# Kernel optimization log

Hardware: AMD Instinct MI355X
Metric: run time of the kernel (lower is better)

Reference implementation:

```python
import jax, jax.numpy as jnp
import numpy as np

DIM = 768
NUM_HEADS = 12
DECAY_RATE = 5.0


def setup_inputs() -> dict:
    key = jax.random.key(0)
    k1, k2, k3, k4 = jax.random.split(key, 4)
    B, N, C = 4, 1024, DIM
    x = jax.random.normal(k1, (B, N, C), dtype=jnp.float32)
    # torch nn.Linear weights: y = x @ W.T ; qkv_bias=False
    qkv_w = jax.random.normal(k2, (3 * C, C), dtype=jnp.float32) * (1.0 / np.sqrt(C))
    proj_w = jax.random.normal(k3, (C, C), dtype=jnp.float32) * (1.0 / np.sqrt(C))
    proj_b = jax.random.normal(k4, (C,), dtype=jnp.float32) * 0.01
    return {"x": x, "qkv_w": qkv_w, "proj_w": proj_w, "proj_b": proj_b, "cur_epoch": 3}


def reference(x, qkv_w, proj_w, proj_b, cur_epoch):
    B, N, C = x.shape
    H = NUM_HEADS
    hd = C // H
    scale = hd ** -0.5

    qkv = (x @ qkv_w.T).reshape(B, N, 3, H, hd).transpose(2, 0, 3, 1, 4)  # [3,B,H,N,hd]
    q, k, v = qkv[0], qkv[1], qkv[2]

    scores = jnp.einsum("bhqd,bhkd->bhqk", q, k) * scale
    logp = jax.nn.log_softmax(scores, axis=-1)
    attn = jnp.exp(logp)  # [B,H,N,N]

    # Per-key entropy: column j of attn flattened over (B,H,N) is renormalized
    # by Categorical; dividing by num_heads cancels under normalization.
    # H(p/s) = log(s) - (1/s) * sum(p * log p)
    s = jnp.sum(attn, axis=(0, 1, 2))                 # [N]
    plogp = jnp.sum(attn * logp, axis=(0, 1, 2))      # [N]
    entropies = jnp.log(s) - plogp / s

    # threshold decay: factor = sum_{i=0}^{cur_epoch-1} decay*exp(-(i+1))
    factor = DECAY_RATE * float(np.sum(np.exp(-(np.arange(cur_epoch) + 1.0))))
    entropy_threshold = float(np.log(C)) - factor

    # attn[:,:,:,keep] @ v[:,:,keep,:] == (attn * mask) @ v  (zeroed columns drop out)
    mask = (entropies <= entropy_threshold).astype(attn.dtype)  # [N]
    out = jnp.einsum("bhqk,bhkd->bhqd", attn * mask[None, None, None, :], v)
    out = out.transpose(0, 2, 1, 3).reshape(B, N, C)
    out = out @ proj_w.T + proj_b
    return out
```

## Files before the change

### kernel.cpp

```cpp
#include <hip/hip_runtime.h>


typedef __bf16 bf16x8 __attribute__((ext_vector_type(8)));
typedef __bf16 bf16x4 __attribute__((ext_vector_type(4)));
typedef float  f32x4  __attribute__((ext_vector_type(4)));

#define MFMA16(a, b, c) __builtin_amdgcn_mfma_f32_16x16x32_bf16((a), (b), (c), 0, 0, 0)
#define LOG2E_8 0.18033688f

__global__ __launch_bounds__(256) void kc_conv(
    const float* __restrict__ x, const float* __restrict__ qw, const float* __restrict__ pw,
    __bf16* __restrict__ xb, __bf16* __restrict__ qwb, __bf16* __restrict__ pwb,
    float* __restrict__ colSP, int* __restrict__ keepCnt)
{
  const int i = blockIdx.x * 256 + threadIdx.x;
  const float4* src;
  __bf16* dst;
  int j;
  if (i < 786432)       { src = (const float4*)x;  dst = xb;  j = i; }
  else if (i < 1228800) { src = (const float4*)qw; dst = qwb; j = i - 786432; }
  else                  { src = (const float4*)pw; dst = pwb; j = i - 1228800; }
  const float4 f = src[j];
  bf16x4 o;
  o[0] = (__bf16)f.x; o[1] = (__bf16)f.y; o[2] = (__bf16)f.z; o[3] = (__bf16)f.w;
  *(bf16x4*)(dst + 4 * (size_t)j) = o;
  if (i < 2048) colSP[i] = 0.f;
  if (i == 0) *keepCnt = 0;
}

__global__ __launch_bounds__(256) void kg_qkv(
    const __bf16* __restrict__ A, const __bf16* __restrict__ Bm,
    __bf16* __restrict__ qb, __bf16* __restrict__ kb, float* __restrict__ v)
{
  __shared__ __bf16 As[64 * 72];
  __shared__ __bf16 Bs[64 * 72];
  const int tid = threadIdx.x;
  const int w = tid >> 6, lane = tid & 63, quad = lane >> 4, l = lane & 15;
  const int r0 = blockIdx.y * 64, c0 = blockIdx.x * 64;
  const int row = tid >> 3, ko = (tid & 7) * 8;
  const f32x4 zero = {0.f, 0.f, 0.f, 0.f};
  f32x4 acc[4];
#pragma unroll
  for (int ct = 0; ct < 4; ++ct) acc[ct] = zero;

  uint4 a0 = *(const uint4*)(A + (size_t)(r0 + row) * 768 + ko);
  uint4 a1 = *(const uint4*)(A + (size_t)(r0 + row + 32) * 768 + ko);
  uint4 b0 = *(const uint4*)(Bm + (size_t)(c0 + row) * 768 + ko);
  uint4 b1 = *(const uint4*)(Bm + (size_t)(c0 + row + 32) * 768 + ko);

  for (int k0 = 0; k0 < 768; k0 += 64) {
    __syncthreads();
    *(uint4*)&As[row * 72 + ko] = a0;
    *(uint4*)&As[(row + 32) * 72 + ko] = a1;
    *(uint4*)&Bs[row * 72 + ko] = b0;
    *(uint4*)&Bs[(row + 32) * 72 + ko] = b1;
    __syncthreads();
    if (k0 < 704) {
      a0 = *(const uint4*)(A + (size_t)(r0 + row) * 768 + k0 + 64 + ko);
      a1 = *(const uint4*)(A + (size_t)(r0 + row + 32) * 768 + k0 + 64 + ko);
      b0 = *(const uint4*)(Bm + (size_t)(c0 + row) * 768 + k0 + 64 + ko);
      b1 = *(const uint4*)(Bm + (size_t)(c0 + row + 32) * 768 + k0 + 64 + ko);
    }
    const bf16x8 af0 = *(const bf16x8*)&As[(w * 16 + l) * 72 + quad * 8];
    const bf16x8 af1 = *(const bf16x8*)&As[(w * 16 + l) * 72 + 32 + quad * 8];
#pragma unroll
    for (int ct = 0; ct < 4; ++ct) {
      const bf16x8 bf0 = *(const bf16x8*)&Bs[(ct * 16 + l) * 72 + quad * 8];
      const bf16x8 bf1 = *(const bf16x8*)&Bs[(ct * 16 + l) * 72 + 32 + quad * 8];
      acc[ct] = MFMA16(af0, bf0, acc[ct]);
      acc[ct] = MFMA16(af1, bf1, acc[ct]);
    }
  }
  const int part = c0 / 768;
  const int h = (c0 % 768) >> 6;
#pragma unroll
  for (int ct = 0; ct < 4; ++ct) {
    const int d = ct * 16 + l;
#pragma unroll
    for (int i = 0; i < 4; ++i) {
      const int rg = r0 + w * 16 + quad * 4 + i;
      const int b_ = rg >> 10, n = rg & 1023;
      const size_t off = ((size_t)(b_ * 12 + h) * 1024 + n) * 64 + d;
      const float val = acc[ct][i];
      if (part == 0)      qb[off] = (__bf16)val;
      else if (part == 1) kb[off] = (__bf16)val;
      else                v[off]  = val;
    }
  }
}

__global__ __launch_bounds__(256) void ks_fused(
    const __bf16* __restrict__ qb, const __bf16* __restrict__ kb,
    float* __restrict__ lse, float* __restrict__ colSP)
{
  __shared__ __bf16 Ks[64 * 72];
  __shared__ float sS[1024];
  __shared__ float sP[1024];
  const int tid = threadIdx.x;
  const int w = tid >> 6, lane = tid & 63, quad = lane >> 4, l = lane & 15;
  const int bh = blockIdx.x, r0 = blockIdx.y * 128;
  const int row = tid >> 3, ko = (tid & 7) * 8;
  for (int i = tid; i < 1024; i += 256) { sS[i] = 0.f; sP[i] = 0.f; }

  const __bf16* qbase = qb + ((size_t)bh * 1024 + r0 + w * 32 + l) * 64;
  bf16x8 aq0[2], aq1[2];
#pragma unroll
  for (int rt = 0; rt < 2; ++rt) {
    aq0[rt] = *(const bf16x8*)(qbase + (size_t)rt * 16 * 64 + quad * 8);
    aq1[rt] = *(const bf16x8*)(qbase + (size_t)rt * 16 * 64 + 32 + quad * 8);
  }
  const __bf16* kbase = kb + (size_t)bh * 65536;
  const f32x4 zero = {0.f, 0.f, 0.f, 0.f};

  uint4 ka0 = *(const uint4*)(kbase + (size_t)row * 64 + ko);
  uint4 ka1 = *(const uint4*)(kbase + (size_t)(row + 32) * 64 + ko);

  float z[8] = {};
  for (int chunk = 0; chunk < 16; ++chunk) {
    __syncthreads();
    *(uint4*)&Ks[row * 72 + ko] = ka0;
    *(uint4*)&Ks[(row + 32) * 72 + ko] = ka1;
    __syncthreads();
    const int nxt = (chunk < 15) ? (chunk + 1) : 0;
    ka0 = *(const uint4*)(kbase + (size_t)(nxt * 64 + row) * 64 + ko);
    ka1 = *(const uint4*)(kbase + (size_t)(nxt * 64 + row + 32) * 64 + ko);
#pragma unroll
    for (int ct = 0; ct < 4; ++ct) {
      const bf16x8 kf0 = *(const bf16x8*)&Ks[(ct * 16 + l) * 72 + quad * 8];
      const bf16x8 kf1 = *(const bf16x8*)&Ks[(ct * 16 + l) * 72 + 32 + quad * 8];
#pragma unroll
      for (int rt = 0; rt < 2; ++rt) {
        f32x4 acc = MFMA16(aq0[rt], kf0, zero);
        acc = MFMA16(aq1[rt], kf1, acc);
#pragma unroll
        for (int r = 0; r < 4; ++r) z[rt * 4 + r] += exp2f(acc[r] * LOG2E_8);
      }
    }
  }
#pragma unroll
  for (int off = 1; off < 16; off <<= 1) {
#pragma unroll
    for (int i = 0; i < 8; ++i) z[i] += __shfl_xor(z[i], off);
  }
  float uu[8], ww[8];
#pragma unroll
  for (int i = 0; i < 8; ++i) {
    const float lg = __logf(z[i]);
    uu[i] = 1.0f / z[i];
    ww[i] = lg * uu[i];
    z[i] = lg;
  }
  if (l == 0) {
#pragma unroll
    for (int rt = 0; rt < 2; ++rt)
#pragma unroll
      for (int r = 0; r < 4; ++r)
        lse[bh * 1024 + r0 + w * 32 + rt * 16 + quad * 4 + r] = z[rt * 4 + r];
  }

  for (int chunk = 0; chunk < 16; ++chunk) {
    __syncthreads();
    *(uint4*)&Ks[row * 72 + ko] = ka0;
    *(uint4*)&Ks[(row + 32) * 72 + ko] = ka1;
    __syncthreads();
    if (chunk < 15) {
      ka0 = *(const uint4*)(kbase + (size_t)((chunk + 1) * 64 + row) * 64 + ko);
      ka1 = *(const uint4*)(kbase + (size_t)((chunk + 1) * 64 + row + 32) * 64 + ko);
    }
#pragma unroll
    for (int ct = 0; ct < 4; ++ct) {
      const bf16x8 kf0 = *(const bf16x8*)&Ks[(ct * 16 + l) * 72 + quad * 8];
      const bf16x8 kf1 = *(const bf16x8*)&Ks[(ct * 16 + l) * 72 + 32 + quad * 8];
      float cs = 0.f, cp = 0.f;
#pragma unroll
      for (int rt = 0; rt < 2; ++rt) {
        f32x4 acc = MFMA16(aq0[rt], kf0, zero);
        acc = MFMA16(aq1[rt], kf1, acc);
#pragma unroll
        for (int r = 0; r < 4; ++r) {
          const float sg = acc[r] * 0.125f;
          const float e = exp2f(acc[r] * LOG2E_8);
          const float t = e * uu[rt * 4 + r];
          cs += t;
          cp += t * sg - e * ww[rt * 4 + r];
        }
      }
      cs += __shfl_xor(cs, 16); cs += __shfl_xor(cs, 32);
      cp += __shfl_xor(cp, 16); cp += __shfl_xor(cp, 32);
      if (lane < 16) {
        atomicAdd(&sS[chunk * 64 + ct * 16 + l], cs);
        atomicAdd(&sP[chunk * 64 + ct * 16 + l], cp);
      }
    }
  }
  __syncthreads();
  for (int i = tid; i < 1024; i += 256) {
    atomicAdd(&colSP[i], sS[i]);
    atomicAdd(&colSP[1024 + i], sP[i]);
  }
}

__global__ void k_mask(const float* __restrict__ colSP, const int* __restrict__ cur_epoch,
                       float* __restrict__ mask, int* __restrict__ keepCnt)
{
  const int j = threadIdx.x;
  const float s = colSP[j];
  const float ent = __logf(s) - colSP[1024 + j] / s;
  const int ce = cur_epoch[0];
  float factor = 0.f;
  for (int i = 1; i <= ce; ++i) factor += __expf(-(float)i);
  factor *= 5.0f;
  const float thr = __logf(768.0f) - factor;
  const int keep = (ent <= thr) ? 1 : 0;
  mask[j] = keep ? 1.0f : 0.0f;
  if (keep) atomicAdd(keepCnt, 1);
}

__global__ __launch_bounds__(256) void k_av(
    const __bf16* __restrict__ qb, const __bf16* __restrict__ kb,
    const float* __restrict__ v, const float* __restrict__ lse,
    const float* __restrict__ mask, const int* __restrict__ keepCnt,
    __bf16* __restrict__ ctxb)
{
  if (*keepCnt == 0) return;
  const int tid = threadIdx.x;
  const int bh = blockIdx.x, r0 = blockIdx.y * 32;
  const int b_ = bh / 12, h = bh % 12;
  __shared__ float qs[32][64];
  __shared__ float pbuf[4][8][64];
  for (int i = tid; i < 2048; i += 256)
    qs[i >> 6][i & 63] = (float)qb[((size_t)bh * 1024 + r0) * 64 + i];
  __syncthreads();
  const int w = tid >> 6, l = tid & 63, rb = w * 8;
  float ls[8];
#pragma unroll
  for (int i = 0; i < 8; ++i) ls[i] = lse[bh * 1024 + r0 + rb + i];
  float acc[8] = {};
  for (int chunk = 0; chunk < 16; ++chunk) {
    const float mk = mask[chunk * 64 + l];
    if (__ballot(mk != 0.0f) == 0ull) continue;
    const __bf16* kp = kb + ((size_t)bh * 1024 + chunk * 64 + l) * 64;
    float s[8] = {};
    for (int d0 = 0; d0 < 64; d0 += 8) {
      const bf16x8 kf = *(const bf16x8*)(kp + d0);
#pragma unroll
      for (int dd = 0; dd < 8; ++dd) {
        const float kv = (float)kf[dd];
#pragma unroll
        for (int i = 0; i < 8; ++i) s[i] += qs[rb + i][d0 + dd] * kv;
      }
    }
    __syncthreads();
#pragma unroll
    for (int i = 0; i < 8; ++i)
      pbuf[w][i][l] = __expf(s[i] * 0.125f - ls[i]) * mk;
    __syncthreads();
    const float* vp = v + ((size_t)bh * 1024 + chunk * 64) * 64 + l;
    for (int jj = 0; jj < 64; ++jj) {
      const float vv = vp[(size_t)jj * 64];
#pragma unroll
      for (int i = 0; i < 8; ++i) acc[i] += pbuf[w][i][jj] * vv;
    }
  }
#pragma unroll
  for (int i = 0; i < 8; ++i)
    ctxb[((size_t)(b_ * 1024 + r0 + rb + i)) * 768 + h * 64 + l] = (__bf16)acc[i];
}

__global__ __launch_bounds__(256) void kg_proj(
    const __bf16* __restrict__ A, const __bf16* __restrict__ Bm,
    const float* __restrict__ bias, const int* __restrict__ keepCnt,
    float* __restrict__ out)
{
  const int tid = threadIdx.x;
  const int w = tid >> 6, lane = tid & 63, quad = lane >> 4, l = lane & 15;
  const int r0 = blockIdx.y * 64, c0 = blockIdx.x * 64;
  if (*keepCnt == 0) {
#pragma unroll
    for (int ct = 0; ct < 4; ++ct) {
      const int c = c0 + ct * 16 + l;
      const float bv = bias[c];
#pragma unroll
      for (int i = 0; i < 4; ++i) {
        const int rg = r0 + w * 16 + quad * 4 + i;
        out[(size_t)rg * 768 + c] = bv;
      }
    }
    return;
  }
  __shared__ __bf16 As[64 * 72];
  __shared__ __bf16 Bs[64 * 72];
  const int row = tid >> 3, ko = (tid & 7) * 8;
  const f32x4 zero = {0.f, 0.f, 0.f, 0.f};
  f32x4 acc[4];
#pragma unroll
  for (int ct = 0; ct < 4; ++ct) acc[ct] = zero;

  uint4 a0 = *(const uint4*)(A + (size_t)(r0 + row) * 768 + ko);
  uint4 a1 = *(const uint4*)(A + (size_t)(r0 + row + 32) * 768 + ko);
  uint4 b0 = *(const uint4*)(Bm + (size_t)(c0 + row) * 768 + ko);
  uint4 b1 = *(const uint4*)(Bm + (size_t)(c0 + row + 32) * 768 + ko);

  for (int k0 = 0; k0 < 768; k0 += 64) {
    __syncthreads();
    *(uint4*)&As[row * 72 + ko] = a0;
    *(uint4*)&As[(row + 32) * 72 + ko] = a1;
    *(uint4*)&Bs[row * 72 + ko] = b0;
    *(uint4*)&Bs[(row + 32) * 72 + ko] = b1;
    __syncthreads();
    if (k0 < 704) {
      a0 = *(const uint4*)(A + (size_t)(r0 + row) * 768 + k0 + 64 + ko);
      a1 = *(const uint4*)(A + (size_t)(r0 + row + 32) * 768 + k0 + 64 + ko);
      b0 = *(const uint4*)(Bm + (size_t)(c0 + row) * 768 + k0 + 64 + ko);
      b1 = *(const uint4*)(Bm + (size_t)(c0 + row + 32) * 768 + k0 + 64 + ko);
    }
    const bf16x8 af0 = *(const bf16x8*)&As[(w * 16 + l) * 72 + quad * 8];
    const bf16x8 af1 = *(const bf16x8*)&As[(w * 16 + l) * 72 + 32 + quad * 8];
#pragma unroll
    for (int ct = 0; ct < 4; ++ct) {
      const bf16x8 bf0 = *(const bf16x8*)&Bs[(ct * 16 + l) * 72 + quad * 8];
      const bf16x8 bf1 = *(const bf16x8*)&Bs[(ct * 16 + l) * 72 + 32 + quad * 8];
      acc[ct] = MFMA16(af0, bf0, acc[ct]);
      acc[ct] = MFMA16(af1, bf1, acc[ct]);
    }
  }
#pragma unroll
  for (int ct = 0; ct < 4; ++ct) {
    const int c = c0 + ct * 16 + l;
#pragma unroll
    for (int i = 0; i < 4; ++i) {
      const int rg = r0 + w * 16 + quad * 4 + i;
      out[(size_t)rg * 768 + c] = acc[ct][i] + bias[c];
    }
  }
}

extern "C" void kernel_launch(void* const* d_in, const int* in_sizes, int n_in,
                              void* d_out, int out_size, void* d_ws, size_t ws_size,
                              hipStream_t stream)
{
  const float* x      = (const float*)d_in[0];
  const float* qkv_w  = (const float*)d_in[1];
  const float* proj_w = (const float*)d_in[2];
  const float* proj_b = (const float*)d_in[3];
  const int*   cur_ep = (const int*)d_in[4];

  char* W = (char*)d_ws;
  __bf16* xb    = (__bf16*)(W + 0);
  __bf16* qwb   = (__bf16*)(W + 6291456);
  __bf16* pwb   = (__bf16*)(W + 9830400);
  __bf16* qb    = (__bf16*)(W + 11010048);
  __bf16* kb    = (__bf16*)(W + 17301504);
  float*  v     = (float*) (W + 23592960);
  __bf16* ctxb  = (__bf16*)(W + 36175872);
  float*  lse   = (float*) (W + 42467328);
  float*  mask  = (float*) (W + 42663936);
  int*    keep  = (int*)   (W + 42668032);
  float*  colSP = (float*) (W + 42668544);
  float*  out   = (float*)d_out;

  kc_conv<<<5376, 256, 0, stream>>>(x, qkv_w, proj_w, xb, qwb, pwb, colSP, keep);
  kg_qkv<<<dim3(36, 64), 256, 0, stream>>>(xb, qwb, qb, kb, v);
  ks_fused<<<dim3(48, 8), 256, 0, stream>>>(qb, kb, lse, colSP);
  k_mask<<<1, 1024, 0, stream>>>(colSP, cur_ep, mask, keep);
  k_av<<<dim3(48, 32), 256, 0, stream>>>(qb, kb, v, lse, mask, keep, ctxb);
  kg_proj<<<dim3(12, 64), 256, 0, stream>>>(ctxb, pwb, proj_b, keep, out);
}
```

Baseline: 185.1 us.

## Split ks_fused work by key slice per wave and double-buffer the K tile

In the score/entropy kernel, each wave now handles one 16-key slice of each 64-key chunk against all 64 query rows of the block, instead of 32 query rows against all keys. Rows per block are halved, which doubles the grid to 768 blocks. The K tile in shared memory is double-buffered, so each iteration needs one barrier instead of two. Per-wave row partial sums are combined through a small shared array with atomics. Column accumulations need no atomics because each wave owns distinct columns. The cost is that K is reloaded by twice as many blocks, plus more registers per thread for the Q fragments and accumulators.

Measured after the change: 166.8 us. -9.9%, faster.

```diff
diff --git a/kernel.cpp b/kernel.cpp
--- a/kernel.cpp
+++ b/kernel.cpp
@@ -93,104 +93,106 @@
     const __bf16* __restrict__ qb, const __bf16* __restrict__ kb,
     float* __restrict__ lse, float* __restrict__ colSP)
 {
-  __shared__ __bf16 Ks[64 * 72];
+  __shared__ __bf16 Ks[2][64 * 72];
   __shared__ float sS[1024];
   __shared__ float sP[1024];
+  __shared__ float zrow[64];
   const int tid = threadIdx.x;
   const int w = tid >> 6, lane = tid & 63, quad = lane >> 4, l = lane & 15;
-  const int bh = blockIdx.x, r0 = blockIdx.y * 128;
+  const int bh = blockIdx.x, r0 = blockIdx.y * 64;
   const int row = tid >> 3, ko = (tid & 7) * 8;
   for (int i = tid; i < 1024; i += 256) { sS[i] = 0.f; sP[i] = 0.f; }
-
-  const __bf16* qbase = qb + ((size_t)bh * 1024 + r0 + w * 32 + l) * 64;
-  bf16x8 aq0[2], aq1[2];
-#pragma unroll
-  for (int rt = 0; rt < 2; ++rt) {
-    aq0[rt] = *(const bf16x8*)(qbase + (size_t)rt * 16 * 64 + quad * 8);
-    aq1[rt] = *(const bf16x8*)(qbase + (size_t)rt * 16 * 64 + 32 + quad * 8);
+  if (tid < 64) zrow[tid] = 0.f;
+
+  const __bf16* qbase = qb + ((size_t)bh * 1024 + r0 + l) * 64;
+  bf16x8 aq0[4], aq1[4];
+#pragma unroll
+  for (int rt = 0; rt < 4; ++rt) {
+    aq0[rt] = *(const bf16x8*)(qbase + rt * 1024 + quad * 8);
+    aq1[rt] = *(const bf16x8*)(qbase + rt * 1024 + 32 + quad * 8);
   }
   const __bf16* kbase = kb + (size_t)bh * 65536;
   const f32x4 zero = {0.f, 0.f, 0.f, 0.f};
+  const int koff = (w * 16 + l) * 72 + quad * 8;
 
   uint4 ka0 = *(const uint4*)(kbase + (size_t)row * 64 + ko);
   uint4 ka1 = *(const uint4*)(kbase + (size_t)(row + 32) * 64 + ko);
 
-  float z[8] = {};
-  for (int chunk = 0; chunk < 16; ++chunk) {
-    __syncthreads();
-    *(uint4*)&Ks[row * 72 + ko] = ka0;
-    *(uint4*)&Ks[(row + 32) * 72 + ko] = ka1;
-    __syncthreads();
-    const int nxt = (chunk < 15) ? (chunk + 1) : 0;
+  float z[16] = {};
+  for (int s = 0; s < 16; ++s) {
+    __bf16* Kw = Ks[s & 1];
+    *(uint4*)&Kw[row * 72 + ko] = ka0;
+    *(uint4*)&Kw[(row + 32) * 72 + ko] = ka1;
+    __syncthreads();
+    const int nxt = (s + 1) & 15;
     ka0 = *(const uint4*)(kbase + (size_t)(nxt * 64 + row) * 64 + ko);
     ka1 = *(const uint4*)(kbase + (size_t)(nxt * 64 + row + 32) * 64 + ko);
-#pragma unroll
-    for (int ct = 0; ct < 4; ++ct) {
-      const bf16x8 kf0 = *(const bf16x8*)&Ks[(ct * 16 + l) * 72 + quad * 8];
-      const bf16x8 kf1 = *(const bf16x8*)&Ks[(ct * 16 + l) * 72 + 32 + quad * 8];
-#pragma unroll
-      for (int rt = 0; rt < 2; ++rt) {
-        f32x4 acc = MFMA16(aq0[rt], kf0, zero);
-        acc = MFMA16(aq1[rt], kf1, acc);
-#pragma unroll
-        for (int r = 0; r < 4; ++r) z[rt * 4 + r] += exp2f(acc[r] * LOG2E_8);
+    const bf16x8 kf0 = *(const bf16x8*)&Kw[koff];
+    const bf16x8 kf1 = *(const bf16x8*)&Kw[koff + 32];
+#pragma unroll
+    for (int rt = 0; rt < 4; ++rt) {
+      f32x4 acc = MFMA16(aq0[rt], kf0, zero);
+      acc = MFMA16(aq1[rt], kf1, acc);
+#pragma unroll
+      for (int r = 0; r < 4; ++r) z[rt * 4 + r] += exp2f(acc[r] * LOG2E_8);
+    }
+  }
+#pragma unroll
+  for (int off = 1; off < 16; off <<= 1) {
+#pragma unroll
+    for (int i = 0; i < 16; ++i) z[i] += __shfl_xor(z[i], off);
+  }
+  if (l == 0) {
+#pragma unroll
+    for (int rt = 0; rt < 4; ++rt)
+#pragma unroll
+      for (int r = 0; r < 4; ++r)
+        atomicAdd(&zrow[rt * 16 + quad * 4 + r], z[rt * 4 + r]);
+  }
+  __syncthreads();
+  if (tid < 64) lse[bh * 1024 + r0 + tid] = __logf(zrow[tid]);
+  float uu[16], ww[16];
+#pragma unroll
+  for (int rt = 0; rt < 4; ++rt) {
+#pragma unroll
+    for (int r = 0; r < 4; ++r) {
+      const float Z = zrow[rt * 16 + quad * 4 + r];
+      const float lg = __logf(Z);
+      uu[rt * 4 + r] = 1.0f / Z;
+      ww[rt * 4 + r] = lg / Z;
+    }
+  }
+
+  for (int s = 0; s < 16; ++s) {
+    __bf16* Kw = Ks[s & 1];
+    *(uint4*)&Kw[row * 72 + ko] = ka0;
+    *(uint4*)&Kw[(row + 32) * 72 + ko] = ka1;
+    __syncthreads();
+    if (s < 15) {
+      ka0 = *(const uint4*)(kbase + (size_t)((s + 1) * 64 + row) * 64 + ko);
+      ka1 = *(const uint4*)(kbase + (size_t)((s + 1) * 64 + row + 32) * 64 + ko);
+    }
+    const bf16x8 kf0 = *(const bf16x8*)&Kw[koff];
+    const bf16x8 kf1 = *(const bf16x8*)&Kw[koff + 32];
+    float cs = 0.f, cp = 0.f;
+#pragma unroll
+    for (int rt = 0; rt < 4; ++rt) {
+      f32x4 acc = MFMA16(aq0[rt], kf0, zero);
+      acc = MFMA16(aq1[rt], kf1, acc);
+#pragma unroll
+      for (int r = 0; r < 4; ++r) {
+        const float sg = acc[r] * 0.125f;
+        const float e = exp2f(acc[r] * LOG2E_8);
+        const float t = e * uu[rt * 4 + r];
+        cs += t;
+        cp += t * sg - e * ww[rt * 4 + r];
       }
     }
-  }
-#pragma unroll
-  for (int off = 1; off < 16; off <<= 1) {
-#pragma unroll
-    for (int i = 0; i < 8; ++i) z[i] += __shfl_xor(z[i], off);
-  }
-  float uu[8], ww[8];
-#pragma unroll
-  for (int i = 0; i < 8; ++i) {
-    const float lg = __logf(z[i]);
-    uu[i] = 1.0f / z[i];
-    ww[i] = lg * uu[i];
-    z[i] = lg;
-  }
-  if (l == 0) {
-#pragma unroll
-    for (int rt = 0; rt < 2; ++rt)
-#pragma unroll
-      for (int r = 0; r < 4; ++r)
-        lse[bh * 1024 + r0 + w * 32 + rt * 16 + quad * 4 + r] = z[rt * 4 + r];
-  }
-
-  for (int chunk = 0; chunk < 16; ++chunk) {
-    __syncthreads();
-    *(uint4*)&Ks[row * 72 + ko] = ka0;
-    *(uint4*)&Ks[(row + 32) * 72 + ko] = ka1;
-    __syncthreads();
-    if (chunk < 15) {
-      ka0 = *(const uint4*)(kbase + (size_t)((chunk + 1) * 64 + row) * 64 + ko);
-      ka1 = *(const uint4*)(kbase + (size_t)((chunk + 1) * 64 + row + 32) * 64 + ko);
-    }
-#pragma unroll
-    for (int ct = 0; ct < 4; ++ct) {
-      const bf16x8 kf0 = *(const bf16x8*)&Ks[(ct * 16 + l) * 72 + quad * 8];
-      const bf16x8 kf1 = *(const bf16x8*)&Ks[(ct * 16 + l) * 72 + 32 + quad * 8];
-      float cs = 0.f, cp = 0.f;
-#pragma unroll
-      for (int rt = 0; rt < 2; ++rt) {
-        f32x4 acc = MFMA16(aq0[rt], kf0, zero);
-        acc = MFMA16(aq1[rt], kf1, acc);
-#pragma unroll
-        for (int r = 0; r < 4; ++r) {
-          const float sg = acc[r] * 0.125f;
-          const float e = exp2f(acc[r] * LOG2E_8);
-          const float t = e * uu[rt * 4 + r];
-          cs += t;
-          cp += t * sg - e * ww[rt * 4 + r];
-        }
-      }
-      cs += __shfl_xor(cs, 16); cs += __shfl_xor(cs, 32);
-      cp += __shfl_xor(cp, 16); cp += __shfl_xor(cp, 32);
-      if (lane < 16) {
-        atomicAdd(&sS[chunk * 64 + ct * 16 + l], cs);
-        atomicAdd(&sP[chunk * 64 + ct * 16 + l], cp);
-      }
+    cs += __shfl_xor(cs, 16); cs += __shfl_xor(cs, 32);
+    cp += __shfl_xor(cp, 16); cp += __shfl_xor(cp, 32);
+    if (lane < 16) {
+      sS[s * 64 + w * 16 + l] += cs;
+      sP[s * 64 + w * 16 + l] += cp;
     }
   }
   __syncthreads();
@@ -361,7 +363,7 @@
 
   kc_conv<<<5376, 256, 0, stream>>>(x, qkv_w, proj_w, xb, qwb, pwb, colSP, keep);
   kg_qkv<<<dim3(36, 64), 256, 0, stream>>>(xb, qwb, qb, kb, v);
-  ks_fused<<<dim3(48, 8), 256, 0, stream>>>(qb, kb, lse, colSP);
+  ks_fused<<<dim3(48, 16), 256, 0, stream>>>(qb, kb, lse, colSP);
   k_mask<<<1, 1024, 0, stream>>>(colSP, cur_ep, mask, keep);
   k_av<<<dim3(48, 32), 256, 0, stream>>>(qb, kb, v, lse, mask, keep, ctxb);
   kg_proj<<<dim3(12, 64), 256, 0, stream>>>(ctxb, pwb, proj_b, keep, out);
```
